# Optimization experiments

Hardware: AMD Instinct MI355X
Metric: run time of the kernel (lower is better)

Reference implementation:

```python
import jax, jax.numpy as jnp
import numpy as np

B, L, H = 16384, 4096, 1024

def setup_inputs() -> dict:
    key = jax.random.key(0)
    k1, k2, k3, k4 = jax.random.split(key, 4)
    return {
        "bert_output": jax.random.normal(k1, (B, H), dtype=jnp.float32),
        "label_embed": jax.random.normal(k2, (L, H), dtype=jnp.float32),
        "W": jax.random.normal(k3, (L, H), dtype=jnp.float32) * (1.0 / np.sqrt(H)),
        "b": jax.random.normal(k4, (L,), dtype=jnp.float32) * 0.02,
    }

def reference(bert_output, label_embed, W, b):
    # Faithful fused form of the original double loop:
    #   logits[i, j] = (W @ (bert_output[i] + label_embed[j]) + b)[j]
    #               = W[j] . bert_output[i] + W[j] . label_embed[j] + b[j]
    # [B,H] @ [H,L] -> [B,L]
    cross = jnp.einsum('bh,lh->bl', bert_output, W)
    # per-label diagonal term: W[j] . label_embed[j]  -> [L]
    label_bias = jnp.einsum('lh,lh->l', W, label_embed) + b
    logits = cross + label_bias[None, :]
    return logits
```

## Files before the change

kernel.cpp:

```cpp
#include <hip/hip_runtime.h>
#include <hip/hip_bf16.h>

constexpr int BDIM = 16384;
constexpr int LDIM = 4096;
constexpr int HDIM = 1024;

constexpr int BM = 256;
constexpr int BN = 128;
constexpr int BK = 64;
constexpr int KTILES = HDIM / BK;

typedef __attribute__((ext_vector_type(4))) int i32x4;

__global__ void prep_kernel(const float* __restrict__ A, const float* __restrict__ W,
                            const float* __restrict__ E, const float* __restrict__ b,
                            signed char* __restrict__ Aq, signed char* __restrict__ Wq,
                            float* __restrict__ sA, float* __restrict__ sW,
                            float* __restrict__ bias) {
  const int bid = blockIdx.x;
  const int w = threadIdx.x >> 6;
  const int l = threadIdx.x & 63;
  const bool isW = bid < (LDIM / 4);
  const int row = isW ? bid * 4 + w : (bid - LDIM / 4) * 4 + w;
  const float4* s4 = (const float4*)((isW ? W : A) + (size_t)row * HDIM);

  float4 v[4];
  float amax = 0.f, dot = 0.f;
#pragma unroll
  for (int i = 0; i < 4; ++i) {
    v[i] = s4[i * 64 + l];
    amax = fmaxf(amax, fmaxf(fmaxf(fabsf(v[i].x), fabsf(v[i].y)),
                             fmaxf(fabsf(v[i].z), fabsf(v[i].w))));
  }
  if (isW) {
    const float4* e4 = (const float4*)(E + (size_t)row * HDIM);
#pragma unroll
    for (int i = 0; i < 4; ++i) {
      float4 ev = e4[i * 64 + l];
      dot += v[i].x * ev.x + v[i].y * ev.y + v[i].z * ev.z + v[i].w * ev.w;
    }
  }
#pragma unroll
  for (int o = 32; o > 0; o >>= 1) amax = fmaxf(amax, __shfl_xor(amax, o, 64));
  if (isW) {
#pragma unroll
    for (int o = 32; o > 0; o >>= 1) dot += __shfl_xor(dot, o, 64);
  }
  const float inv = amax > 0.f ? 127.f / amax : 0.f;
  unsigned int* dst = (unsigned int*)((isW ? Wq : Aq) + (size_t)row * HDIM);
#pragma unroll
  for (int i = 0; i < 4; ++i) {
    int q0 = (int)rintf(v[i].x * inv), q1 = (int)rintf(v[i].y * inv);
    int q2 = (int)rintf(v[i].z * inv), q3 = (int)rintf(v[i].w * inv);
    dst[i * 64 + l] =
        (q0 & 255) | ((q1 & 255) << 8) | ((q2 & 255) << 16) | ((q3 & 255) << 24);
  }
  if (l == 0) {
    if (isW) { sW[row] = amax * (1.f / 127.f); bias[row] = dot + b[row]; }
    else sA[row] = amax * (1.f / 127.f);
  }
}

__device__ __forceinline__ void gld_lds16(const void* g, void* l) {
  __builtin_amdgcn_global_load_lds(
      (const __attribute__((address_space(1))) void*)g,
      (__attribute__((address_space(3))) void*)l, 16, 0, 0);
}

#define MEMPIN asm volatile("" ::: "memory")
#define SCHED0 __builtin_amdgcn_sched_barrier(0)
#define BAR __builtin_amdgcn_s_barrier()
#define LGKM0 asm volatile("s_waitcnt lgkmcnt(0)" ::: "memory")
#define VM1 asm volatile("s_waitcnt vmcnt(1)" ::: "memory")
#define VM0 asm volatile("s_waitcnt vmcnt(0)" ::: "memory")
#define VMNONE (void)0

__global__ __launch_bounds__(512, 4) void gemm_kernel(
    const signed char* __restrict__ Aq,
    const signed char* __restrict__ Wq,
    const float* __restrict__ sA,
    const float* __restrict__ sW,
    const float* __restrict__ bias,
    float* __restrict__ C)
{
  __shared__ __attribute__((aligned(128))) signed char As[2 * BM * BK];
  __shared__ __attribute__((aligned(128))) signed char Bs[4 * BN * BK];

  const int tid = threadIdx.x;
  const int w = tid >> 6;
  const int l = tid & 63;
  const int wr = w >> 1;
  const int wc = w & 1;
  const int lr = l & 15;
  const int hi = l >> 4;

  const int bid = blockIdx.x;
  const int swz = (bid & 7) * 256 + (bid >> 3);
  const int mblk = swz >> 5;
  const int nblk = swz & 31;
  const int brow = mblk * BM;
  const int bcol = nblk * BN;

  const int srow = tid >> 2;
  const int scn = (tid & 3) ^ ((tid >> 3) & 3);
  const signed char* aSrc = Aq + (size_t)(brow + srow) * HDIM + scn * 16;
  const signed char* bSrc = Wq + (size_t)(bcol + srow) * HDIM + scn * 16;

  const int c0 = (hi ^ ((lr >> 1) & 3)) * 16;
  const int rowA = wr * 64 + lr;
  const int rowB = wc * 64 + lr;

  i32x4 acc[4][4] = {};
  i32x4 aF[4], bF[4];

#define ISSUE_A(d, kk)                                                         \
  { const signed char* s_ = aSrc + (kk) * BK;                                  \
    gld_lds16(s_, &As[(d) * 16384 + w * 1024]);                                \
    gld_lds16(s_ + (size_t)128 * HDIM, &As[(d) * 16384 + 8192 + w * 1024]); }
#define ISSUE_B(s, kk)                                                         \
  gld_lds16(bSrc + (kk) * BK, &Bs[(s) * 8192 + w * 1024]);

#define READ_AB(d, s)                                                          \
  _Pragma("unroll") for (int mi = 0; mi < 4; ++mi)                             \
    aF[mi] = *(const i32x4*)&As[(d) * 16384 + (rowA + mi * 16) * 64 + c0];     \
  _Pragma("unroll") for (int ni = 0; ni < 4; ++ni)                             \
    bF[ni] = *(const i32x4*)&Bs[(s) * 8192 + (rowB + ni * 16) * 64 + c0];

#define MFMA16                                                                 \
  _Pragma("unroll") for (int mi = 0; mi < 4; ++mi) {                           \
    _Pragma("unroll") for (int ni = 0; ni < 4; ++ni) {                         \
      acc[mi][ni] = __builtin_amdgcn_mfma_i32_16x16x64_i8(                     \
          aF[mi], bF[ni], acc[mi][ni], 0, 0, 0);                               \
    }                                                                          \
  }

#define TILE(d, s, SA, tA, SB, sB, tB, VMW, DOBAR)                             \
  { READ_AB(d, s)                                                              \
    if (SA) ISSUE_A((d) ^ 1, (tA));                                            \
    SCHED0; LGKM0; SCHED0;                                                     \
    __builtin_amdgcn_s_setprio(1);                                             \
    MFMA16                                                                     \
    __builtin_amdgcn_s_setprio(0);                                             \
    SCHED0;                                                                    \
    if (SB) ISSUE_B((sB), (tB));                                               \
    VMW; MEMPIN;                                                               \
    if (DOBAR) BAR;                                                            \
    MEMPIN; }

  ISSUE_A(0, 0); ISSUE_B(0, 0); ISSUE_B(1, 1);
  VM1;
  MEMPIN; BAR;

#pragma unroll 1
  for (int t = 0; t < 12; t += 4) {
    TILE(0, 0, 1, t + 1, 1, 2, t + 2, VM1, 1);
    TILE(1, 1, 1, t + 2, 1, 3, t + 3, VM1, 1);
    TILE(0, 2, 1, t + 3, 1, 0, t + 4, VM1, 1);
    TILE(1, 3, 1, t + 4, 1, 1, t + 5, VM1, 1);
  }
  TILE(0, 0, 1, 13, 1, 2, 14, VM1, 1);
  TILE(1, 1, 1, 14, 1, 3, 15, VM1, 1);
  TILE(0, 2, 1, 15, 0, 0, 0, VM0, 1);
  TILE(1, 3, 0, 0, 0, 0, 0, VMNONE, 0);

  float sw4[4], bv[4];
#pragma unroll
  for (int ni = 0; ni < 4; ++ni) {
    const int cc = bcol + wc * 64 + ni * 16 + lr;
    sw4[ni] = sW[cc];
    bv[ni] = bias[cc];
  }
  const int orow0 = brow + wr * 64 + hi * 4;
  const int ocol0 = bcol + wc * 64 + lr;
#pragma unroll
  for (int mi = 0; mi < 4; ++mi) {
#pragma unroll
    for (int r = 0; r < 4; ++r) {
      const float sa = sA[orow0 + mi * 16 + r];
#pragma unroll
      for (int ni = 0; ni < 4; ++ni) {
        C[(size_t)(orow0 + mi * 16 + r) * LDIM + ocol0 + ni * 16] =
            (float)acc[mi][ni][r] * (sa * sw4[ni]) + bv[ni];
      }
    }
  }
#undef TILE
#undef MFMA16
#undef READ_AB
#undef ISSUE_A
#undef ISSUE_B
}

extern "C" void kernel_launch(void* const* d_in, const int* in_sizes, int n_in,
                              void* d_out, int out_size, void* d_ws, size_t ws_size,
                              hipStream_t stream) {
  const float* bert = (const float*)d_in[0];
  const float* emb  = (const float*)d_in[1];
  const float* W    = (const float*)d_in[2];
  const float* b    = (const float*)d_in[3];
  float* out = (float*)d_out;

  char* ws = (char*)d_ws;
  signed char* Aq = (signed char*)ws;
  signed char* Wq = (signed char*)(ws + (size_t)BDIM * HDIM);
  float* sAp  = (float*)(ws + (size_t)BDIM * HDIM + (size_t)LDIM * HDIM);
  float* sWp  = (float*)((char*)sAp + BDIM * sizeof(float));
  float* bias = (float*)((char*)sWp + LDIM * sizeof(float));

  hipLaunchKernelGGL(prep_kernel, dim3(LDIM / 4 + BDIM / 4), dim3(256), 0, stream,
                     bert, W, emb, b, Aq, Wq, sAp, sWp, bias);
  hipLaunchKernelGGL(gemm_kernel, dim3((BDIM / BM) * (LDIM / BN)), dim3(512), 0, stream,
                     Aq, Wq, sAp, sWp, bias, out);
}
```

Baseline: 136.0 us.

## Use 256x256 block tile with 32x32x32 int8 MFMA and 4-stage ring

Doubles the block N tile to 256 and splits the 8 waves as 2x4, each computing 128x64 with the 32x32x32 int8 MFMA instead of 16x16x64. A and B now both use a 4-slot LDS ring with loads issued two k-tiles ahead, and each k-tile is split into two half-K phases separated by barriers. The aim is more data reuse per LDS byte and fewer MFMA issues. In exchange it needs more LDS and registers, occupancy drops to 2 blocks per CU, there are more barriers per k-tile, and the grid halves to 1024 blocks.

```diff
diff --git a/kernel.cpp b/kernel.cpp
--- a/kernel.cpp
+++ b/kernel.cpp
@@ -6,11 +6,12 @@
 constexpr int HDIM = 1024;
 
 constexpr int BM = 256;
-constexpr int BN = 128;
+constexpr int BN = 256;
 constexpr int BK = 64;
 constexpr int KTILES = HDIM / BK;
 
 typedef __attribute__((ext_vector_type(4))) int i32x4;
+typedef __attribute__((ext_vector_type(16))) int i32x16;
 
 __global__ void prep_kernel(const float* __restrict__ A, const float* __restrict__ W,
                             const float* __restrict__ E, const float* __restrict__ b,
@@ -71,11 +72,11 @@
 #define SCHED0 __builtin_amdgcn_sched_barrier(0)
 #define BAR __builtin_amdgcn_s_barrier()
 #define LGKM0 asm volatile("s_waitcnt lgkmcnt(0)" ::: "memory")
-#define VM1 asm volatile("s_waitcnt vmcnt(1)" ::: "memory")
+#define VM4 asm volatile("s_waitcnt vmcnt(4)" ::: "memory")
 #define VM0 asm volatile("s_waitcnt vmcnt(0)" ::: "memory")
 #define VMNONE (void)0
 
-__global__ __launch_bounds__(512, 4) void gemm_kernel(
+__global__ __launch_bounds__(512, 2) void gemm_kernel(
     const signed char* __restrict__ Aq,
     const signed char* __restrict__ Wq,
     const float* __restrict__ sA,
@@ -83,21 +84,21 @@
     const float* __restrict__ bias,
     float* __restrict__ C)
 {
-  __shared__ __attribute__((aligned(128))) signed char As[2 * BM * BK];
+  __shared__ __attribute__((aligned(128))) signed char As[4 * BM * BK];
   __shared__ __attribute__((aligned(128))) signed char Bs[4 * BN * BK];
 
   const int tid = threadIdx.x;
   const int w = tid >> 6;
   const int l = tid & 63;
-  const int wr = w >> 1;
-  const int wc = w & 1;
-  const int lr = l & 15;
-  const int hi = l >> 4;
+  const int wr = w >> 2;
+  const int wc = w & 3;
+  const int l31 = l & 31;
+  const int hi5 = l >> 5;
 
   const int bid = blockIdx.x;
-  const int swz = (bid & 7) * 256 + (bid >> 3);
-  const int mblk = swz >> 5;
-  const int nblk = swz & 31;
+  const int swz = (bid & 7) * 128 + (bid >> 3);
+  const int mblk = swz >> 4;
+  const int nblk = swz & 15;
   const int brow = mblk * BM;
   const int bcol = nblk * BN;
 
@@ -105,88 +106,96 @@
   const int scn = (tid & 3) ^ ((tid >> 3) & 3);
   const signed char* aSrc = Aq + (size_t)(brow + srow) * HDIM + scn * 16;
   const signed char* bSrc = Wq + (size_t)(bcol + srow) * HDIM + scn * 16;
-
-  const int c0 = (hi ^ ((lr >> 1) & 3)) * 16;
-  const int rowA = wr * 64 + lr;
-  const int rowB = wc * 64 + lr;
-
-  i32x4 acc[4][4] = {};
-  i32x4 aF[4], bF[4];
-
-#define ISSUE_A(d, kk)                                                         \
+  const int wdst = w * 1024;
+
+  const int csw = (l31 >> 1) & 3;
+  const int c0 = ((0 + hi5) ^ csw) * 16;
+  const int c1 = ((2 + hi5) ^ csw) * 16;
+
+  i32x16 acc[4][2] = {};
+  i32x4 aF0[4], aF1[4], bF0[2], bF1[2];
+
+#define ISSUE_A(s, kk)                                                         \
   { const signed char* s_ = aSrc + (kk) * BK;                                  \
-    gld_lds16(s_, &As[(d) * 16384 + w * 1024]);                                \
-    gld_lds16(s_ + (size_t)128 * HDIM, &As[(d) * 16384 + 8192 + w * 1024]); }
+    gld_lds16(s_, &As[(s) * 16384 + wdst]);                                    \
+    gld_lds16(s_ + (size_t)128 * HDIM, &As[(s) * 16384 + 8192 + wdst]); }
 #define ISSUE_B(s, kk)                                                         \
-  gld_lds16(bSrc + (kk) * BK, &Bs[(s) * 8192 + w * 1024]);
-
-#define READ_AB(d, s)                                                          \
-  _Pragma("unroll") for (int mi = 0; mi < 4; ++mi)                             \
-    aF[mi] = *(const i32x4*)&As[(d) * 16384 + (rowA + mi * 16) * 64 + c0];     \
-  _Pragma("unroll") for (int ni = 0; ni < 4; ++ni)                             \
-    bF[ni] = *(const i32x4*)&Bs[(s) * 8192 + (rowB + ni * 16) * 64 + c0];
-
-#define MFMA16                                                                 \
-  _Pragma("unroll") for (int mi = 0; mi < 4; ++mi) {                           \
-    _Pragma("unroll") for (int ni = 0; ni < 4; ++ni) {                         \
-      acc[mi][ni] = __builtin_amdgcn_mfma_i32_16x16x64_i8(                     \
-          aF[mi], bF[ni], acc[mi][ni], 0, 0, 0);                               \
+  { const signed char* s_ = bSrc + (kk) * BK;                                  \
+    gld_lds16(s_, &Bs[(s) * 16384 + wdst]);                                    \
+    gld_lds16(s_ + (size_t)128 * HDIM, &Bs[(s) * 16384 + 8192 + wdst]); }
+
+#define READ6(s, CC, AF, BF)                                                   \
+  _Pragma("unroll") for (int mf = 0; mf < 4; ++mf)                             \
+    AF[mf] = *(const i32x4*)&As[(s) * 16384 +                                  \
+                                (wr * 128 + mf * 32 + l31) * 64 + (CC)];       \
+  _Pragma("unroll") for (int nf = 0; nf < 2; ++nf)                             \
+    BF[nf] = *(const i32x4*)&Bs[(s) * 16384 +                                  \
+                                (wc * 64 + nf * 32 + l31) * 64 + (CC)];
+
+#define MFMA8(AF, BF)                                                          \
+  _Pragma("unroll") for (int mf = 0; mf < 4; ++mf) {                           \
+    _Pragma("unroll") for (int nf = 0; nf < 2; ++nf) {                         \
+      acc[mf][nf] = __builtin_amdgcn_mfma_i32_32x32x32_i8(                     \
+          AF[mf], BF[nf], acc[mf][nf], 0, 0, 0);                               \
     }                                                                          \
   }
 
-#define TILE(d, s, SA, tA, SB, sB, tB, VMW, DOBAR)                             \
-  { READ_AB(d, s)                                                              \
-    if (SA) ISSUE_A((d) ^ 1, (tA));                                            \
-    SCHED0; LGKM0; SCHED0;                                                     \
+#define TILE(s, s2, SA, SB, tk2, VMW)                                          \
+  { READ6(s, c0, aF0, bF0)                                                     \
+    if (SA) ISSUE_A((s2), (tk2));                                              \
+    MEMPIN; BAR; LGKM0; SCHED0;                                                \
     __builtin_amdgcn_s_setprio(1);                                             \
-    MFMA16                                                                     \
+    MFMA8(aF0, bF0)                                                            \
     __builtin_amdgcn_s_setprio(0);                                             \
     SCHED0;                                                                    \
-    if (SB) ISSUE_B((sB), (tB));                                               \
-    VMW; MEMPIN;                                                               \
-    if (DOBAR) BAR;                                                            \
-    MEMPIN; }
-
-  ISSUE_A(0, 0); ISSUE_B(0, 0); ISSUE_B(1, 1);
-  VM1;
+    READ6(s, c1, aF1, bF1)                                                     \
+    if (SB) ISSUE_B((s2), (tk2));                                              \
+    MEMPIN; BAR; LGKM0; SCHED0;                                                \
+    __builtin_amdgcn_s_setprio(1);                                             \
+    MFMA8(aF1, bF1)                                                            \
+    __builtin_amdgcn_s_setprio(0);                                             \
+    SCHED0;                                                                    \
+    VMW; MEMPIN; }
+
+  ISSUE_A(0, 0); ISSUE_B(0, 0); ISSUE_A(1, 1); ISSUE_B(1, 1);
+  VM4;
   MEMPIN; BAR;
 
 #pragma unroll 1
   for (int t = 0; t < 12; t += 4) {
-    TILE(0, 0, 1, t + 1, 1, 2, t + 2, VM1, 1);
-    TILE(1, 1, 1, t + 2, 1, 3, t + 3, VM1, 1);
-    TILE(0, 2, 1, t + 3, 1, 0, t + 4, VM1, 1);
-    TILE(1, 3, 1, t + 4, 1, 1, t + 5, VM1, 1);
-  }
-  TILE(0, 0, 1, 13, 1, 2, 14, VM1, 1);
-  TILE(1, 1, 1, 14, 1, 3, 15, VM1, 1);
-  TILE(0, 2, 1, 15, 0, 0, 0, VM0, 1);
-  TILE(1, 3, 0, 0, 0, 0, 0, VMNONE, 0);
-
-  float sw4[4], bv[4];
-#pragma unroll
-  for (int ni = 0; ni < 4; ++ni) {
-    const int cc = bcol + wc * 64 + ni * 16 + lr;
-    sw4[ni] = sW[cc];
-    bv[ni] = bias[cc];
-  }
-  const int orow0 = brow + wr * 64 + hi * 4;
-  const int ocol0 = bcol + wc * 64 + lr;
-#pragma unroll
-  for (int mi = 0; mi < 4; ++mi) {
-#pragma unroll
-    for (int r = 0; r < 4; ++r) {
-      const float sa = sA[orow0 + mi * 16 + r];
-#pragma unroll
-      for (int ni = 0; ni < 4; ++ni) {
-        C[(size_t)(orow0 + mi * 16 + r) * LDIM + ocol0 + ni * 16] =
-            (float)acc[mi][ni][r] * (sa * sw4[ni]) + bv[ni];
-      }
+    TILE(0, 2, 1, 1, t + 2, VM4);
+    TILE(1, 3, 1, 1, t + 3, VM4);
+    TILE(2, 0, 1, 1, t + 4, VM4);
+    TILE(3, 1, 1, 1, t + 5, VM4);
+  }
+  TILE(0, 2, 1, 1, 14, VM4);
+  TILE(1, 3, 1, 1, 15, VM4);
+  TILE(2, 0, 0, 0, 0, VM0);
+  TILE(3, 1, 0, 0, 0, VMNONE);
+
+  float sw2[2], bv2[2];
+#pragma unroll
+  for (int nf = 0; nf < 2; ++nf) {
+    const int cc = bcol + wc * 64 + nf * 32 + l31;
+    sw2[nf] = sW[cc];
+    bv2[nf] = bias[cc];
+  }
+  const int ocol = bcol + wc * 64 + l31;
+#pragma unroll
+  for (int mf = 0; mf < 4; ++mf) {
+    const int rb = brow + wr * 128 + mf * 32 + hi5 * 4;
+#pragma unroll
+    for (int reg = 0; reg < 16; ++reg) {
+      const int row = rb + (reg & 3) + 8 * (reg >> 2);
+      const float sa = sA[row];
+      const size_t off = (size_t)row * LDIM + ocol;
+      C[off]      = (float)acc[mf][0][reg] * (sa * sw2[0]) + bv2[0];
+      C[off + 32] = (float)acc[mf][1][reg] * (sa * sw2[1]) + bv2[1];
     }
   }
 #undef TILE
-#undef MFMA16
-#undef READ_AB
+#undef MFMA8
+#undef READ6
 #undef ISSUE_A
 #undef ISSUE_B
 }
```

Measured after the change: 151.9 us. +11.7%, slower.

## Stage GEMM epilogue through LDS for coalesced float4 stores and remap block order

Applied to the files above, without the earlier changes.

The epilogue now writes scaled accumulators into a padded LDS tile, four row-chunks at a time, then reads them back as float4 so each wave stores full contiguous row segments of C instead of scattered 4-byte writes. The two shared arrays are merged into one 64KB buffer that is reused for this staging. The block-to-tile mapping also changes so that consecutive blocks cover different M blocks while sharing N columns. The staging adds extra barriers and LDS traffic at the end of every block, and the new swizzle may change L2 reuse of A and W tiles.

```diff
diff --git a/kernel.cpp b/kernel.cpp
--- a/kernel.cpp
+++ b/kernel.cpp
@@ -83,8 +83,9 @@
     const float* __restrict__ bias,
     float* __restrict__ C)
 {
-  __shared__ __attribute__((aligned(128))) signed char As[2 * BM * BK];
-  __shared__ __attribute__((aligned(128))) signed char Bs[4 * BN * BK];
+  __shared__ __attribute__((aligned(128))) signed char LDSU[65536];
+  signed char* As = LDSU;
+  signed char* Bs = LDSU + 32768;
 
   const int tid = threadIdx.x;
   const int w = tid >> 6;
@@ -95,9 +96,8 @@
   const int hi = l >> 4;
 
   const int bid = blockIdx.x;
-  const int swz = (bid & 7) * 256 + (bid >> 3);
-  const int mblk = swz >> 5;
-  const int nblk = swz & 31;
+  const int mblk = (bid & 7) * 8 + (bid >> 8);
+  const int nblk = (bid >> 3) & 31;
   const int brow = mblk * BM;
   const int bcol = nblk * BN;
 
@@ -170,19 +170,32 @@
     sw4[ni] = sW[cc];
     bv[ni] = bias[cc];
   }
-  const int orow0 = brow + wr * 64 + hi * 4;
-  const int ocol0 = bcol + wc * 64 + lr;
-#pragma unroll
-  for (int mi = 0; mi < 4; ++mi) {
+  MEMPIN; BAR;
+  float* T = (float*)LDSU;
+
+#pragma unroll
+  for (int c = 0; c < 4; ++c) {
 #pragma unroll
     for (int r = 0; r < 4; ++r) {
-      const float sa = sA[orow0 + mi * 16 + r];
+      const int grow = brow + wr * 64 + c * 16 + hi * 4 + r;
+      const float sa = sA[grow];
+      const int trow = wr * 16 + hi * 4 + r;
 #pragma unroll
       for (int ni = 0; ni < 4; ++ni) {
-        C[(size_t)(orow0 + mi * 16 + r) * LDIM + ocol0 + ni * 16] =
-            (float)acc[mi][ni][r] * (sa * sw4[ni]) + bv[ni];
+        T[trow * 132 + wc * 64 + ni * 16 + lr] =
+            (float)acc[c][ni][r] * (sa * sw4[ni]) + bv[ni];
       }
     }
+    MEMPIN; BAR;
+#pragma unroll
+    for (int k = 0; k < 4; ++k) {
+      const int u = w * 64 + l + k * 512;
+      const int row = u >> 5, c4 = u & 31;
+      const int grow = brow + (row >> 4) * 64 + c * 16 + (row & 15);
+      float4 v = *(const float4*)&T[row * 132 + c4 * 4];
+      *(float4*)&C[(size_t)grow * LDIM + bcol + c4 * 4] = v;
+    }
+    MEMPIN; BAR;
   }
 #undef TILE
 #undef MFMA16
```

Result: no change. 137.5 us (+1.2%).

## Switch GEMM to unified 3-stage A/B LDS pipeline with prefetch distance two

Applied to the files above, without the earlier changes.

Restructures the int8 GEMM software pipeline. A was double-buffered and B quad-buffered; both now use a shared 3-stage LDS ring, and A and B for tile k+2 are issued together before the MFMAs. The vmcnt wait becomes 3 so two tiles stay in flight. This aims to hide more global-load latency for A. LDS use rises from 64KB to 72KB per block, which may reduce occupancy at 4 blocks per CU.

```diff
diff --git a/kernel.cpp b/kernel.cpp
--- a/kernel.cpp
+++ b/kernel.cpp
@@ -71,7 +71,7 @@
 #define SCHED0 __builtin_amdgcn_sched_barrier(0)
 #define BAR __builtin_amdgcn_s_barrier()
 #define LGKM0 asm volatile("s_waitcnt lgkmcnt(0)" ::: "memory")
-#define VM1 asm volatile("s_waitcnt vmcnt(1)" ::: "memory")
+#define VM3 asm volatile("s_waitcnt vmcnt(3)" ::: "memory")
 #define VM0 asm volatile("s_waitcnt vmcnt(0)" ::: "memory")
 #define VMNONE (void)0
 
@@ -83,8 +83,8 @@
     const float* __restrict__ bias,
     float* __restrict__ C)
 {
-  __shared__ __attribute__((aligned(128))) signed char As[2 * BM * BK];
-  __shared__ __attribute__((aligned(128))) signed char Bs[4 * BN * BK];
+  __shared__ __attribute__((aligned(128))) signed char As[3 * BM * BK];
+  __shared__ __attribute__((aligned(128))) signed char Bs[3 * BN * BK];
 
   const int tid = threadIdx.x;
   const int w = tid >> 6;
@@ -113,16 +113,16 @@
   i32x4 acc[4][4] = {};
   i32x4 aF[4], bF[4];
 
-#define ISSUE_A(d, kk)                                                         \
+#define ISSUE_A(s, kk)                                                         \
   { const signed char* s_ = aSrc + (kk) * BK;                                  \
-    gld_lds16(s_, &As[(d) * 16384 + w * 1024]);                                \
-    gld_lds16(s_ + (size_t)128 * HDIM, &As[(d) * 16384 + 8192 + w * 1024]); }
+    gld_lds16(s_, &As[(s) * 16384 + w * 1024]);                                \
+    gld_lds16(s_ + (size_t)128 * HDIM, &As[(s) * 16384 + 8192 + w * 1024]); }
 #define ISSUE_B(s, kk)                                                         \
   gld_lds16(bSrc + (kk) * BK, &Bs[(s) * 8192 + w * 1024]);
 
-#define READ_AB(d, s)                                                          \
+#define READ_AB(s)                                                             \
   _Pragma("unroll") for (int mi = 0; mi < 4; ++mi)                             \
-    aF[mi] = *(const i32x4*)&As[(d) * 16384 + (rowA + mi * 16) * 64 + c0];     \
+    aF[mi] = *(const i32x4*)&As[(s) * 16384 + (rowA + mi * 16) * 64 + c0];     \
   _Pragma("unroll") for (int ni = 0; ni < 4; ++ni)                             \
     bF[ni] = *(const i32x4*)&Bs[(s) * 8192 + (rowB + ni * 16) * 64 + c0];
 
@@ -134,34 +134,32 @@
     }                                                                          \
   }
 
-#define TILE(d, s, SA, tA, SB, sB, tB, VMW, DOBAR)                             \
-  { READ_AB(d, s)                                                              \
-    if (SA) ISSUE_A((d) ^ 1, (tA));                                            \
+#define TILE(s, s2, SS, tk2, VMW, DOBAR)                                       \
+  { READ_AB(s)                                                                 \
+    if (SS) { ISSUE_A((s2), (tk2)); ISSUE_B((s2), (tk2)); }                    \
     SCHED0; LGKM0; SCHED0;                                                     \
     __builtin_amdgcn_s_setprio(1);                                             \
     MFMA16                                                                     \
     __builtin_amdgcn_s_setprio(0);                                             \
     SCHED0;                                                                    \
-    if (SB) ISSUE_B((sB), (tB));                                               \
     VMW; MEMPIN;                                                               \
     if (DOBAR) BAR;                                                            \
     MEMPIN; }
 
-  ISSUE_A(0, 0); ISSUE_B(0, 0); ISSUE_B(1, 1);
-  VM1;
+  ISSUE_A(0, 0); ISSUE_B(0, 0); ISSUE_A(1, 1); ISSUE_B(1, 1);
+  VM3;
   MEMPIN; BAR;
 
 #pragma unroll 1
-  for (int t = 0; t < 12; t += 4) {
-    TILE(0, 0, 1, t + 1, 1, 2, t + 2, VM1, 1);
-    TILE(1, 1, 1, t + 2, 1, 3, t + 3, VM1, 1);
-    TILE(0, 2, 1, t + 3, 1, 0, t + 4, VM1, 1);
-    TILE(1, 3, 1, t + 4, 1, 1, t + 5, VM1, 1);
-  }
-  TILE(0, 0, 1, 13, 1, 2, 14, VM1, 1);
-  TILE(1, 1, 1, 14, 1, 3, 15, VM1, 1);
-  TILE(0, 2, 1, 15, 0, 0, 0, VM0, 1);
-  TILE(1, 3, 0, 0, 0, 0, 0, VMNONE, 0);
+  for (int t = 0; t < 12; t += 3) {
+    TILE(0, 2, 1, t + 2, VM3, 1);
+    TILE(1, 0, 1, t + 3, VM3, 1);
+    TILE(2, 1, 1, t + 4, VM3, 1);
+  }
+  TILE(0, 2, 1, 14, VM3, 1);
+  TILE(1, 0, 1, 15, VM3, 1);
+  TILE(2, 0, 0, 0, VM0, 1);
+  TILE(0, 0, 0, 0, VMNONE, 0);
 
   float sw4[4], bv[4];
 #pragma unroll
```

Measured after the change: 136.5 us. Within noise of the previous version (+0.4%).
